# Kernel optimization log

Hardware: AMD Instinct MI355X
Metric: run time of the kernel (lower is better)

## Reference

```python
import jax, jax.numpy as jnp
import numpy as np

B, Q, H, NH, HD = 2, 1024, 2048, 16, 128
QKV_ALPHA = 1e-4   # W8A8B8O8Linear output scale (a)
QKV_BETA = 1.0     # W8A8B8O8Linear bias scale (b)
QK_SCALE = 1e-4    # BMM_S8T_S8N_F32T dequant scale
PV_SCALE = 2e-3    # BMM_S8T_S8N_S8T output scale
DENSE_ALPHA = 1e-5 # W8A8BFP32OFP32Linear dequant scale
INV_NORM = 1.0 / (HD ** 0.5)


def setup_inputs() -> dict:
    key = jax.random.key(0)
    ks = jax.random.split(key, 8)
    hidden_states = jax.random.randint(ks[0], (B, Q, H), -128, 128, dtype=jnp.int32)  # int8 activations
    residual = jax.random.normal(ks[1], (B, Q, H), dtype=jnp.float32)
    alibi = jax.random.normal(ks[2], (B * NH, 1, Q), dtype=jnp.float32) * 0.1
    causal = jnp.triu(jnp.ones((Q, Q), dtype=bool), k=1)  # True = masked (future positions)
    attention_mask = jnp.broadcast_to(causal[None, None], (B, 1, Q, Q))
    w_qkv = jax.random.randint(ks[3], (3 * H, H), -128, 128, dtype=jnp.int32)   # int8 weight
    b_qkv = jax.random.randint(ks[4], (3 * H,), -128, 128, dtype=jnp.int32)     # int8 bias
    w_dense = jax.random.randint(ks[5], (H, H), -128, 128, dtype=jnp.int32)     # int8 weight
    b_dense = jax.random.normal(ks[6], (H,), dtype=jnp.float32)                 # fp32 bias
    return dict(hidden_states=hidden_states, residual=residual, alibi=alibi,
                attention_mask=attention_mask, w_qkv=w_qkv, b_qkv=b_qkv,
                w_dense=w_dense, b_dense=b_dense)


def _quant_i8(x_f32):
    return jnp.clip(jnp.round(x_f32), -128, 127).astype(jnp.int32)


def reference(hidden_states, residual, alibi, attention_mask, w_qkv, b_qkv, w_dense, b_dense):
    # --- W8A8B8O8 fused QKV linear: int8 in, int8 out ---
    acc = jnp.einsum('bqh,oh->bqo', hidden_states, w_qkv)  # exact int32 accumulation
    fused_qkv = _quant_i8(acc.astype(jnp.float32) * QKV_ALPHA + b_qkv.astype(jnp.float32) * QKV_BETA)
    # _split_heads: [B,Q,3H] -> [B,Q,NH,3,HD]
    qkv = fused_qkv.reshape(B, Q, NH, 3, HD)
    q = qkv[..., 0, :].transpose(0, 2, 1, 3).reshape(B * NH, Q, HD)
    k = qkv[..., 1, :].transpose(0, 2, 1, 3).reshape(B * NH, Q, HD)
    v = qkv[..., 2, :].transpose(0, 2, 1, 3).reshape(B * NH, Q, HD)
    # --- BMM_S8T_S8N_F32T: int8 q @ k^T -> fp32 * scale, plus alibi bias ---
    scores_i32 = jnp.einsum('nqd,nkd->nqk', q, k)  # [B*NH,Q,KV] int32
    matmul_result = alibi * 1.0 + scores_i32.astype(jnp.float32) * QK_SCALE * INV_NORM
    attention_scores = matmul_result.reshape(B, NH, Q, Q)
    # masked softmax (True = masked)
    attn_weights = jnp.where(attention_mask, jnp.finfo(jnp.float32).min, attention_scores)
    attention_probs = jax.nn.softmax(attn_weights, axis=-1)
    # quantize probs to int8 with scale 1/127 (BMM_S8T_S8N_S8T A-side)
    p_i8 = _quant_i8(attention_probs * 127.0).reshape(B * NH, Q, Q)
    # --- BMM_S8T_S8N_S8T: int8 probs @ int8 v -> int8 context ---
    ctx_acc = jnp.einsum('nqk,nkd->nqd', p_i8, v)  # int32
    ctx_i8 = _quant_i8(ctx_acc.astype(jnp.float32) * PV_SCALE)
    # _merge_heads: [B*NH,Q,HD] -> [B,Q,H]
    ctx = ctx_i8.reshape(B, NH, Q, HD).transpose(0, 2, 1, 3).reshape(B, Q, H)
    # --- W8A8BFP32OFP32 dense: int8 in, fp32 out ---
    dense_acc = jnp.einsum('bqh,oh->bqo', ctx, w_dense)
    output = dense_acc.astype(jnp.float32) * DENSE_ALPHA + b_dense + residual
    return output
```

## Files before the change

### kernel.cpp

```cpp
#include <hip/hip_runtime.h>
#include <stdint.h>

typedef int i32x4 __attribute__((ext_vector_type(4)));

#define DEV __device__ __forceinline__

DEV void glds16(const void* g, void* l) {
  __builtin_amdgcn_global_load_lds(
      (const __attribute__((address_space(1))) void*)g,
      (__attribute__((address_space(3))) void*)l, 16, 0, 0);
}

DEV int clampi8(float f) {
  int v = (int)rintf(f);
  return v < -128 ? -128 : (v > 127 ? 127 : v);
}

__global__ void pack_kernel(const int* __restrict__ src, int8_t* __restrict__ dst, int n4) {
  int i = blockIdx.x * blockDim.x + threadIdx.x;
  if (i < n4) {
    int4 v = ((const int4*)src)[i];
    char4 c;
    c.x = (char)v.x; c.y = (char)v.y; c.z = (char)v.z; c.w = (char)v.w;
    ((char4*)dst)[i] = c;
  }
}

template<int K>
DEV void gemm_core(const int8_t* __restrict__ A, const int8_t* __restrict__ B,
                   int row0, int col0, i32x4 acc[4][4], char* lA, char* lB,
                   int l, int w, int wm, int wn) {
  const int lr = l & 15, lg = l >> 4;
  for (int k0 = 0; k0 < K; k0 += 64) {
    __syncthreads();
#pragma unroll
    for (int t = 0; t < 2; ++t) {
      const int mb = w * 2 + t;
      glds16(A + (size_t)(row0 + mb * 16 + lr) * K + k0 + lg * 16, lA + mb * 1024);
      glds16(B + (size_t)(col0 + mb * 16 + lr) * K + k0 + lg * 16, lB + mb * 1024);
    }
    __syncthreads();
    i32x4 a[4], b[4];
#pragma unroll
    for (int i = 0; i < 4; ++i) a[i] = *(const i32x4*)(lA + ((wm * 4 + i) * 64 + l) * 16);
#pragma unroll
    for (int j = 0; j < 4; ++j) b[j] = *(const i32x4*)(lB + ((wn * 4 + j) * 64 + l) * 16);
#pragma unroll
    for (int i = 0; i < 4; ++i)
#pragma unroll
      for (int j = 0; j < 4; ++j)
        acc[i][j] = __builtin_amdgcn_mfma_i32_16x16x64_i8(a[i], b[j], acc[i][j], 0, 0, 0);
  }
}

__global__ __launch_bounds__(256) void qkv_kernel(
    const int8_t* __restrict__ hs8, const int8_t* __restrict__ w8,
    const int* __restrict__ bq, int8_t* __restrict__ qb, int8_t* __restrict__ kb,
    int8_t* __restrict__ vT) {
  __shared__ __align__(16) char lA[8192];
  __shared__ __align__(16) char lB[8192];
  const int l = threadIdx.x & 63, w = threadIdx.x >> 6;
  const int wm = w >> 1, wn = w & 1;
  const int lr = l & 15, lg = l >> 4;
  const int row0 = blockIdx.y * 128, col0 = blockIdx.x * 128;
  i32x4 acc[4][4] = {};
  gemm_core<2048>(hs8, w8, row0, col0, acc, lA, lB, l, w, wm, wn);
#pragma unroll
  for (int j = 0; j < 4; ++j) {
    const int col = col0 + (wn * 4 + j) * 16 + lr;
    const float bias = (float)bq[col];
    const int nh = col / 384, rem = col - nh * 384;
    const int s = rem >> 7, d = rem & 127;
#pragma unroll
    for (int i = 0; i < 4; ++i) {
#pragma unroll
      for (int r = 0; r < 4; ++r) {
        const int row = row0 + (wm * 4 + i) * 16 + lg * 4 + r;
        const int bb = row >> 10, qpos = row & 1023;
        const int n = bb * 16 + nh;
        const int8_t c = (int8_t)clampi8((float)acc[i][j][r] * 1e-4f + bias);
        if (s == 0)      qb[((size_t)n << 17) + (qpos << 7) + d] = c;
        else if (s == 1) kb[((size_t)n << 17) + (qpos << 7) + d] = c;
        else             vT[((size_t)n << 17) + (d << 10) + qpos] = c;
      }
    }
  }
}

__global__ __launch_bounds__(256) void attn_stats_kernel(
    const int8_t* __restrict__ qb, const int8_t* __restrict__ kb,
    const float* __restrict__ alibi, float* __restrict__ stats) {
  __shared__ __align__(16) char lQ[16384];
  __shared__ __align__(16) char lK[16384];
  const int n = blockIdx.y;
  const int tri = blockIdx.x;
  int qt = 0;
  while ((qt + 1) * (qt + 2) / 2 <= tri) ++qt;
  const int kt = tri - qt * (qt + 1) / 2;
  const int l = threadIdx.x & 63, w = threadIdx.x >> 6;
  const int lr = l & 15, lg = l >> 4;
  const int row0 = qt * 128;
  const int8_t* Qh = qb + ((size_t)n << 17);
  const int8_t* Kh = kb + ((size_t)n << 17);
  const float* al = alibi + n * 1024;

#pragma unroll
  for (int e0 = 0; e0 < 4; ++e0) {
    const int e = w * 4 + e0, ks = e >> 3, mb = e & 7;
    glds16(Qh + (size_t)(row0 + mb * 16 + lr) * 128 + ks * 64 + lg * 16, lQ + e * 1024);
    glds16(Kh + (size_t)(kt * 128 + mb * 16 + lr) * 128 + ks * 64 + lg * 16, lK + e * 1024);
  }
  __syncthreads();
  i32x4 qa[2][2];
#pragma unroll
  for (int t = 0; t < 2; ++t)
#pragma unroll
    for (int ks = 0; ks < 2; ++ks)
      qa[t][ks] = *(const i32x4*)(lQ + (ks * 8 + w * 2 + t) * 1024 + l * 16);

  float sf[2][8][4];
#pragma unroll
  for (int nf = 0; nf < 8; ++nf) {
    const i32x4 bk0 = *(const i32x4*)(lK + nf * 1024 + l * 16);
    const i32x4 bk1 = *(const i32x4*)(lK + (8 + nf) * 1024 + l * 16);
    const int col = kt * 128 + nf * 16 + lr;
    const float av = al[col];
#pragma unroll
    for (int t = 0; t < 2; ++t) {
      i32x4 sa = {0, 0, 0, 0};
      sa = __builtin_amdgcn_mfma_i32_16x16x64_i8(qa[t][0], bk0, sa, 0, 0, 0);
      sa = __builtin_amdgcn_mfma_i32_16x16x64_i8(qa[t][1], bk1, sa, 0, 0, 0);
#pragma unroll
      for (int r = 0; r < 4; ++r) {
        const int rowg = row0 + (w * 2 + t) * 16 + lg * 4 + r;
        sf[t][nf][r] = (col <= rowg)
            ? av + ((float)sa[r] * 1e-4f) * 0.08838834764831843f
            : -INFINITY;
      }
    }
  }
#pragma unroll
  for (int t = 0; t < 2; ++t)
#pragma unroll
    for (int r = 0; r < 4; ++r) {
      float tm = sf[t][0][r];
#pragma unroll
      for (int nf = 1; nf < 8; ++nf) tm = fmaxf(tm, sf[t][nf][r]);
#pragma unroll
      for (int o = 1; o < 16; o <<= 1) tm = fmaxf(tm, __shfl_xor(tm, o));
      float es = 0.f;
#pragma unroll
      for (int nf = 0; nf < 8; ++nf) es += __expf(sf[t][nf][r] - tm);
#pragma unroll
      for (int o = 1; o < 16; o <<= 1) es += __shfl_xor(es, o);
      if (lr == 0) {
        const int rowl = (w * 2 + t) * 16 + lg * 4 + r;
        float2* st = (float2*)stats;
        st[((n * 8 + qt) * 8 + kt) * 128 + rowl] = make_float2(tm, es);
      }
    }
}

__global__ __launch_bounds__(256) void attn_pv_kernel(
    const int8_t* __restrict__ qb, const int8_t* __restrict__ kb,
    const int8_t* __restrict__ vT, const float* __restrict__ alibi,
    const float* __restrict__ stats, int* __restrict__ slab0,
    int* __restrict__ slab1, int8_t* __restrict__ ctx) {
  __shared__ __align__(16) char lQ[16384];
  __shared__ __align__(16) char lK[16384];
  __shared__ __align__(16) char lV[16384];
  __shared__ __align__(16) char lP[128 * 144];
  const int n = blockIdx.y, gi = blockIdx.x;
  int qt, g, kt0, kt1;
  if (gi < 4) { qt = gi; g = 0; kt0 = 0; kt1 = qt + 1; }
  else { const int p = gi - 4; qt = 4 + (p >> 1); g = p & 1; kt0 = g ? 4 : 0; kt1 = g ? qt + 1 : 4; }
  const int l = threadIdx.x & 63, w = threadIdx.x >> 6;
  const int lr = l & 15, lg = l >> 4;
  const int row0 = qt * 128;
  const int8_t* Qh = qb + ((size_t)n << 17);
  const int8_t* Kh = kb + ((size_t)n << 17);
  const int8_t* Vh = vT + ((size_t)n << 17);
  const float* al = alibi + n * 1024;

#pragma unroll
  for (int e0 = 0; e0 < 4; ++e0) {
    const int e = w * 4 + e0, ks = e >> 3, mb = e & 7;
    glds16(Qh + (size_t)(row0 + mb * 16 + lr) * 128 + ks * 64 + lg * 16, lQ + e * 1024);
  }
  __syncthreads();
  i32x4 qa[2][2];
#pragma unroll
  for (int t = 0; t < 2; ++t)
#pragma unroll
    for (int ks = 0; ks < 2; ++ks)
      qa[t][ks] = *(const i32x4*)(lQ + (ks * 8 + w * 2 + t) * 1024 + l * 16);

  float mrow[2][4], srow[2][4];
  const float2* st = (const float2*)stats;
#pragma unroll
  for (int t = 0; t < 2; ++t)
#pragma unroll
    for (int r = 0; r < 4; ++r) {
      const int rowl = (w * 2 + t) * 16 + lg * 4 + r;
      const int base = ((n * 8 + qt) * 8) * 128 + rowl;
      float m = -INFINITY;
      for (int k2 = 0; k2 <= qt; ++k2) m = fmaxf(m, st[base + k2 * 128].x);
      float s = 0.f;
      for (int k2 = 0; k2 <= qt; ++k2) {
        const float2 p = st[base + k2 * 128];
        s += p.y * __expf(p.x - m);
      }
      mrow[t][r] = m; srow[t][r] = s;
    }

  i32x4 pacc[2][8] = {};
  for (int kt = kt0; kt < kt1; ++kt) {
    __syncthreads();
#pragma unroll
    for (int e0 = 0; e0 < 4; ++e0) {
      const int e = w * 4 + e0, ks = e >> 3, mb = e & 7;
      glds16(Kh + (size_t)(kt * 128 + mb * 16 + lr) * 128 + ks * 64 + lg * 16, lK + e * 1024);
      glds16(Vh + (size_t)(mb * 16 + lr) * 1024 + kt * 128 + ks * 64 + lg * 16, lV + e * 1024);
    }
    __syncthreads();
#pragma unroll
    for (int nf = 0; nf < 8; ++nf) {
      const i32x4 bk0 = *(const i32x4*)(lK + nf * 1024 + l * 16);
      const i32x4 bk1 = *(const i32x4*)(lK + (8 + nf) * 1024 + l * 16);
      const int col = kt * 128 + nf * 16 + lr;
      const float av = al[col];
#pragma unroll
      for (int t = 0; t < 2; ++t) {
        i32x4 sa = {0, 0, 0, 0};
        sa = __builtin_amdgcn_mfma_i32_16x16x64_i8(qa[t][0], bk0, sa, 0, 0, 0);
        sa = __builtin_amdgcn_mfma_i32_16x16x64_i8(qa[t][1], bk1, sa, 0, 0, 0);
#pragma unroll
        for (int r = 0; r < 4; ++r) {
          const int rowl = (w * 2 + t) * 16 + lg * 4 + r;
          const int rowg = row0 + rowl;
          int p = 0;
          if (col <= rowg) {
            const float s = av + ((float)sa[r] * 1e-4f) * 0.08838834764831843f;
            p = (int)rintf(__expf(s - mrow[t][r]) / srow[t][r] * 127.0f);
          }
          lP[rowl * 144 + nf * 16 + lr] = (char)p;
        }
      }
    }
    __syncthreads();
#pragma unroll
    for (int t = 0; t < 2; ++t) {
      const int rowl = (w * 2 + t) * 16 + lr;
      const i32x4 pa0 = *(const i32x4*)(lP + rowl * 144 + lg * 16);
      const i32x4 pa1 = *(const i32x4*)(lP + rowl * 144 + 64 + lg * 16);
#pragma unroll
      for (int nf = 0; nf < 8; ++nf) {
        const i32x4 vb0 = *(const i32x4*)(lV + nf * 1024 + l * 16);
        const i32x4 vb1 = *(const i32x4*)(lV + (8 + nf) * 1024 + l * 16);
        pacc[t][nf] = __builtin_amdgcn_mfma_i32_16x16x64_i8(pa0, vb0, pacc[t][nf], 0, 0, 0);
        pacc[t][nf] = __builtin_amdgcn_mfma_i32_16x16x64_i8(pa1, vb1, pacc[t][nf], 0, 0, 0);
      }
    }
  }
  const int bb = n >> 4, nh = n & 15;
  if (qt < 4) {
#pragma unroll
    for (int t = 0; t < 2; ++t)
#pragma unroll
      for (int nf = 0; nf < 8; ++nf)
#pragma unroll
        for (int r = 0; r < 4; ++r) {
          const int qpos = row0 + (w * 2 + t) * 16 + lg * 4 + r;
          const int d = nf * 16 + lr;
          ctx[((size_t)(bb * 1024 + qpos)) * 2048 + nh * 128 + d] =
              (int8_t)clampi8((float)pacc[t][nf][r] * 2e-3f);
        }
  } else {
    int* slab = g ? slab1 : slab0;
#pragma unroll
    for (int t = 0; t < 2; ++t)
#pragma unroll
      for (int nf = 0; nf < 8; ++nf)
#pragma unroll
        for (int r = 0; r < 4; ++r) {
          const int qpos = row0 + (w * 2 + t) * 16 + lg * 4 + r;
          const int d = nf * 16 + lr;
          slab[(size_t)(bb * 512 + qpos - 512) * 2048 + nh * 128 + d] = pacc[t][nf][r];
        }
  }
}

__global__ void ctx_reduce_kernel(const int* __restrict__ slab0,
                                  const int* __restrict__ slab1,
                                  int8_t* __restrict__ ctx) {
  const int i = blockIdx.x * blockDim.x + threadIdx.x;
  const int4 a = ((const int4*)slab0)[i];
  const int4 b = ((const int4*)slab1)[i];
  const int elem0 = i * 4;
  const int r512 = elem0 >> 11, col = elem0 & 2047;
  const int bb = r512 >> 9, qpos = 512 + (r512 & 511);
  char4 c;
  c.x = (char)clampi8((float)(a.x + b.x) * 2e-3f);
  c.y = (char)clampi8((float)(a.y + b.y) * 2e-3f);
  c.z = (char)clampi8((float)(a.z + b.z) * 2e-3f);
  c.w = (char)clampi8((float)(a.w + b.w) * 2e-3f);
  ((char4*)ctx)[((size_t)(bb * 1024 + qpos) * 2048 + col) >> 2] = c;
}

__global__ __launch_bounds__(256) void dense_kernel(
    const int8_t* __restrict__ c8, const int8_t* __restrict__ w8,
    const float* __restrict__ bd, const float* __restrict__ res,
    float* __restrict__ out) {
  __shared__ __align__(16) char lA[8192];
  __shared__ __align__(16) char lB[8192];
  const int l = threadIdx.x & 63, w = threadIdx.x >> 6;
  const int wm = w >> 1, wn = w & 1;
  const int lr = l & 15, lg = l >> 4;
  const int row0 = blockIdx.y * 128, col0 = blockIdx.x * 128;
  i32x4 acc[4][4] = {};
  gemm_core<2048>(c8, w8, row0, col0, acc, lA, lB, l, w, wm, wn);
#pragma unroll
  for (int j = 0; j < 4; ++j) {
    const int col = col0 + (wn * 4 + j) * 16 + lr;
    const float bias = bd[col];
#pragma unroll
    for (int i = 0; i < 4; ++i) {
#pragma unroll
      for (int r = 0; r < 4; ++r) {
        const int row = row0 + (wm * 4 + i) * 16 + lg * 4 + r;
        const size_t o = (size_t)row * 2048 + col;
        out[o] = (float)acc[i][j][r] * 1e-5f + bias + res[o];
      }
    }
  }
}

extern "C" void kernel_launch(void* const* d_in, const int* in_sizes, int n_in,
                              void* d_out, int out_size, void* d_ws, size_t ws_size,
                              hipStream_t stream) {
  const int* hs = (const int*)d_in[0];
  const float* res = (const float*)d_in[1];
  const float* alibi = (const float*)d_in[2];
  const int* wqkv = (const int*)d_in[4];
  const int* bqkv = (const int*)d_in[5];
  const int* wd = (const int*)d_in[6];
  const float* bd = (const float*)d_in[7];
  float* out = (float*)d_out;
  char* ws = (char*)d_ws;

  int8_t* hs8   = (int8_t*)(ws + 0);
  int8_t* wqkv8 = (int8_t*)(ws + 4194304);
  int*    slab0 = (int*)(ws + 0);
  int*    slab1 = (int*)(ws + 8388608);
  int8_t* wd8   = (int8_t*)(ws + 16777216);
  int8_t* q8b   = (int8_t*)(ws + 20971520);
  int8_t* k8b   = (int8_t*)(ws + 25165824);
  int8_t* vT8   = (int8_t*)(ws + 29360128);
  int8_t* ctx8  = (int8_t*)(ws + 33554432);
  float*  stats = (float*)(ws + 37748736);

  pack_kernel<<<4096, 256, 0, stream>>>(hs, hs8, 1048576);
  pack_kernel<<<12288, 256, 0, stream>>>(wqkv, wqkv8, 3145728);
  pack_kernel<<<4096, 256, 0, stream>>>(wd, wd8, 1048576);
  qkv_kernel<<<dim3(48, 16), 256, 0, stream>>>(hs8, wqkv8, bqkv, q8b, k8b, vT8);
  attn_stats_kernel<<<dim3(36, 32), 256, 0, stream>>>(q8b, k8b, alibi, stats);
  attn_pv_kernel<<<dim3(12, 32), 256, 0, stream>>>(q8b, k8b, vT8, alibi, stats,
                                                   slab0, slab1, ctx8);
  ctx_reduce_kernel<<<2048, 256, 0, stream>>>(slab0, slab1, ctx8);
  dense_kernel<<<dim3(16, 16), 256, 0, stream>>>(ctx8, wd8, bd, res, out);
}
```

Baseline: 189.5 us.

## Double-buffer GEMM loads, fuse pack kernels, drop LDS staging in attention

The shared GEMM core now double-buffers its LDS tiles: it prefetches the next K-slice with global_load_lds while computing on the current one, leaving one barrier per iteration instead of two. The dense GEMM moves to a 128x64 tile with its own double-buffered loop, giving twice as many blocks. The three int32-to-int8 pack launches merge into one kernel. The attention kernels load Q, K and V fragments straight from global memory into registers instead of staging them through LDS. That removes barriers and LDS traffic but relies on cache hits for the repeated strided reads.

```diff
diff --git a/kernel.cpp b/kernel.cpp
--- a/kernel.cpp
+++ b/kernel.cpp
@@ -16,14 +16,20 @@
   return v < -128 ? -128 : (v > 127 ? 127 : v);
 }
 
-__global__ void pack_kernel(const int* __restrict__ src, int8_t* __restrict__ dst, int n4) {
-  int i = blockIdx.x * blockDim.x + threadIdx.x;
-  if (i < n4) {
-    int4 v = ((const int4*)src)[i];
-    char4 c;
-    c.x = (char)v.x; c.y = (char)v.y; c.z = (char)v.z; c.w = (char)v.w;
-    ((char4*)dst)[i] = c;
-  }
+__global__ void pack_all_kernel(const int* __restrict__ s0, const int* __restrict__ s1,
+                                const int* __restrict__ s2, int8_t* __restrict__ d0,
+                                int8_t* __restrict__ d1, int8_t* __restrict__ d2) {
+  const int i = blockIdx.x * 256 + threadIdx.x;
+  const int* s;
+  int8_t* d;
+  int j;
+  if (i < 1048576) { s = s0; d = d0; j = i; }
+  else if (i < 4194304) { s = s1; d = d1; j = i - 1048576; }
+  else { s = s2; d = d2; j = i - 4194304; }
+  int4 v = ((const int4*)s)[j];
+  char4 c;
+  c.x = (char)v.x; c.y = (char)v.y; c.z = (char)v.z; c.w = (char)v.w;
+  ((char4*)d)[j] = c;
 }
 
 template<int K>
@@ -31,25 +37,38 @@
                    int row0, int col0, i32x4 acc[4][4], char* lA, char* lB,
                    int l, int w, int wm, int wn) {
   const int lr = l & 15, lg = l >> 4;
+  const int8_t* pA0 = A + (size_t)(row0 + (w * 2 + 0) * 16 + lr) * K + lg * 16;
+  const int8_t* pA1 = A + (size_t)(row0 + (w * 2 + 1) * 16 + lr) * K + lg * 16;
+  const int8_t* pB0 = B + (size_t)(col0 + (w * 2 + 0) * 16 + lr) * K + lg * 16;
+  const int8_t* pB1 = B + (size_t)(col0 + (w * 2 + 1) * 16 + lr) * K + lg * 16;
+  glds16(pA0, lA + (w * 2 + 0) * 1024);
+  glds16(pA1, lA + (w * 2 + 1) * 1024);
+  glds16(pB0, lB + (w * 2 + 0) * 1024);
+  glds16(pB1, lB + (w * 2 + 1) * 1024);
+  __syncthreads();
+  int cur = 0;
   for (int k0 = 0; k0 < K; k0 += 64) {
-    __syncthreads();
-#pragma unroll
-    for (int t = 0; t < 2; ++t) {
-      const int mb = w * 2 + t;
-      glds16(A + (size_t)(row0 + mb * 16 + lr) * K + k0 + lg * 16, lA + mb * 1024);
-      glds16(B + (size_t)(col0 + mb * 16 + lr) * K + k0 + lg * 16, lB + mb * 1024);
-    }
-    __syncthreads();
+    const int nxt = cur ^ 1;
+    if (k0 + 64 < K) {
+      glds16(pA0 + k0 + 64, lA + nxt * 8192 + (w * 2 + 0) * 1024);
+      glds16(pA1 + k0 + 64, lA + nxt * 8192 + (w * 2 + 1) * 1024);
+      glds16(pB0 + k0 + 64, lB + nxt * 8192 + (w * 2 + 0) * 1024);
+      glds16(pB1 + k0 + 64, lB + nxt * 8192 + (w * 2 + 1) * 1024);
+    }
     i32x4 a[4], b[4];
 #pragma unroll
-    for (int i = 0; i < 4; ++i) a[i] = *(const i32x4*)(lA + ((wm * 4 + i) * 64 + l) * 16);
-#pragma unroll
-    for (int j = 0; j < 4; ++j) b[j] = *(const i32x4*)(lB + ((wn * 4 + j) * 64 + l) * 16);
+    for (int i = 0; i < 4; ++i)
+      a[i] = *(const i32x4*)(lA + cur * 8192 + ((wm * 4 + i) * 64 + l) * 16);
+#pragma unroll
+    for (int j = 0; j < 4; ++j)
+      b[j] = *(const i32x4*)(lB + cur * 8192 + ((wn * 4 + j) * 64 + l) * 16);
 #pragma unroll
     for (int i = 0; i < 4; ++i)
 #pragma unroll
       for (int j = 0; j < 4; ++j)
         acc[i][j] = __builtin_amdgcn_mfma_i32_16x16x64_i8(a[i], b[j], acc[i][j], 0, 0, 0);
+    __syncthreads();
+    cur = nxt;
   }
 }
 
@@ -57,8 +76,8 @@
     const int8_t* __restrict__ hs8, const int8_t* __restrict__ w8,
     const int* __restrict__ bq, int8_t* __restrict__ qb, int8_t* __restrict__ kb,
     int8_t* __restrict__ vT) {
-  __shared__ __align__(16) char lA[8192];
-  __shared__ __align__(16) char lB[8192];
+  __shared__ __align__(16) char lA[16384];
+  __shared__ __align__(16) char lB[16384];
   const int l = threadIdx.x & 63, w = threadIdx.x >> 6;
   const int wm = w >> 1, wn = w & 1;
   const int lr = l & 15, lg = l >> 4;
@@ -90,8 +109,6 @@
 __global__ __launch_bounds__(256) void attn_stats_kernel(
     const int8_t* __restrict__ qb, const int8_t* __restrict__ kb,
     const float* __restrict__ alibi, float* __restrict__ stats) {
-  __shared__ __align__(16) char lQ[16384];
-  __shared__ __align__(16) char lK[16384];
   const int n = blockIdx.y;
   const int tri = blockIdx.x;
   int qt = 0;
@@ -104,25 +121,19 @@
   const int8_t* Kh = kb + ((size_t)n << 17);
   const float* al = alibi + n * 1024;
 
-#pragma unroll
-  for (int e0 = 0; e0 < 4; ++e0) {
-    const int e = w * 4 + e0, ks = e >> 3, mb = e & 7;
-    glds16(Qh + (size_t)(row0 + mb * 16 + lr) * 128 + ks * 64 + lg * 16, lQ + e * 1024);
-    glds16(Kh + (size_t)(kt * 128 + mb * 16 + lr) * 128 + ks * 64 + lg * 16, lK + e * 1024);
-  }
-  __syncthreads();
   i32x4 qa[2][2];
 #pragma unroll
   for (int t = 0; t < 2; ++t)
 #pragma unroll
     for (int ks = 0; ks < 2; ++ks)
-      qa[t][ks] = *(const i32x4*)(lQ + (ks * 8 + w * 2 + t) * 1024 + l * 16);
+      qa[t][ks] = *(const i32x4*)(Qh + (size_t)(row0 + (w * 2 + t) * 16 + lr) * 128 + ks * 64 + lg * 16);
 
   float sf[2][8][4];
 #pragma unroll
   for (int nf = 0; nf < 8; ++nf) {
-    const i32x4 bk0 = *(const i32x4*)(lK + nf * 1024 + l * 16);
-    const i32x4 bk1 = *(const i32x4*)(lK + (8 + nf) * 1024 + l * 16);
+    const size_t krow = (size_t)(kt * 128 + nf * 16 + lr) * 128;
+    const i32x4 bk0 = *(const i32x4*)(Kh + krow + lg * 16);
+    const i32x4 bk1 = *(const i32x4*)(Kh + krow + 64 + lg * 16);
     const int col = kt * 128 + nf * 16 + lr;
     const float av = al[col];
 #pragma unroll
@@ -166,9 +177,6 @@
     const int8_t* __restrict__ vT, const float* __restrict__ alibi,
     const float* __restrict__ stats, int* __restrict__ slab0,
     int* __restrict__ slab1, int8_t* __restrict__ ctx) {
-  __shared__ __align__(16) char lQ[16384];
-  __shared__ __align__(16) char lK[16384];
-  __shared__ __align__(16) char lV[16384];
   __shared__ __align__(16) char lP[128 * 144];
   const int n = blockIdx.y, gi = blockIdx.x;
   int qt, g, kt0, kt1;
@@ -182,18 +190,12 @@
   const int8_t* Vh = vT + ((size_t)n << 17);
   const float* al = alibi + n * 1024;
 
-#pragma unroll
-  for (int e0 = 0; e0 < 4; ++e0) {
-    const int e = w * 4 + e0, ks = e >> 3, mb = e & 7;
-    glds16(Qh + (size_t)(row0 + mb * 16 + lr) * 128 + ks * 64 + lg * 16, lQ + e * 1024);
-  }
-  __syncthreads();
   i32x4 qa[2][2];
 #pragma unroll
   for (int t = 0; t < 2; ++t)
 #pragma unroll
     for (int ks = 0; ks < 2; ++ks)
-      qa[t][ks] = *(const i32x4*)(lQ + (ks * 8 + w * 2 + t) * 1024 + l * 16);
+      qa[t][ks] = *(const i32x4*)(Qh + (size_t)(row0 + (w * 2 + t) * 16 + lr) * 128 + ks * 64 + lg * 16);
 
   float mrow[2][4], srow[2][4];
   const float2* st = (const float2*)stats;
@@ -215,18 +217,11 @@
 
   i32x4 pacc[2][8] = {};
   for (int kt = kt0; kt < kt1; ++kt) {
-    __syncthreads();
-#pragma unroll
-    for (int e0 = 0; e0 < 4; ++e0) {
-      const int e = w * 4 + e0, ks = e >> 3, mb = e & 7;
-      glds16(Kh + (size_t)(kt * 128 + mb * 16 + lr) * 128 + ks * 64 + lg * 16, lK + e * 1024);
-      glds16(Vh + (size_t)(mb * 16 + lr) * 1024 + kt * 128 + ks * 64 + lg * 16, lV + e * 1024);
-    }
-    __syncthreads();
 #pragma unroll
     for (int nf = 0; nf < 8; ++nf) {
-      const i32x4 bk0 = *(const i32x4*)(lK + nf * 1024 + l * 16);
-      const i32x4 bk1 = *(const i32x4*)(lK + (8 + nf) * 1024 + l * 16);
+      const size_t krow = (size_t)(kt * 128 + nf * 16 + lr) * 128;
+      const i32x4 bk0 = *(const i32x4*)(Kh + krow + lg * 16);
+      const i32x4 bk1 = *(const i32x4*)(Kh + krow + 64 + lg * 16);
       const int col = kt * 128 + nf * 16 + lr;
       const float av = al[col];
 #pragma unroll
@@ -255,8 +250,9 @@
       const i32x4 pa1 = *(const i32x4*)(lP + rowl * 144 + 64 + lg * 16);
 #pragma unroll
       for (int nf = 0; nf < 8; ++nf) {
-        const i32x4 vb0 = *(const i32x4*)(lV + nf * 1024 + l * 16);
-        const i32x4 vb1 = *(const i32x4*)(lV + (8 + nf) * 1024 + l * 16);
+        const size_t vrow = (size_t)(nf * 16 + lr) * 1024 + kt * 128;
+        const i32x4 vb0 = *(const i32x4*)(Vh + vrow + lg * 16);
+        const i32x4 vb1 = *(const i32x4*)(Vh + vrow + 64 + lg * 16);
         pacc[t][nf] = __builtin_amdgcn_mfma_i32_16x16x64_i8(pa0, vb0, pacc[t][nf], 0, 0, 0);
         pacc[t][nf] = __builtin_amdgcn_mfma_i32_16x16x64_i8(pa1, vb1, pacc[t][nf], 0, 0, 0);
       }
@@ -311,17 +307,46 @@
     const int8_t* __restrict__ c8, const int8_t* __restrict__ w8,
     const float* __restrict__ bd, const float* __restrict__ res,
     float* __restrict__ out) {
-  __shared__ __align__(16) char lA[8192];
+  __shared__ __align__(16) char lA[16384];
   __shared__ __align__(16) char lB[8192];
   const int l = threadIdx.x & 63, w = threadIdx.x >> 6;
   const int wm = w >> 1, wn = w & 1;
   const int lr = l & 15, lg = l >> 4;
-  const int row0 = blockIdx.y * 128, col0 = blockIdx.x * 128;
-  i32x4 acc[4][4] = {};
-  gemm_core<2048>(c8, w8, row0, col0, acc, lA, lB, l, w, wm, wn);
-#pragma unroll
-  for (int j = 0; j < 4; ++j) {
-    const int col = col0 + (wn * 4 + j) * 16 + lr;
+  const int row0 = blockIdx.y * 128, col0 = blockIdx.x * 64;
+  const int8_t* pA0 = c8 + (size_t)(row0 + (w * 2 + 0) * 16 + lr) * 2048 + lg * 16;
+  const int8_t* pA1 = c8 + (size_t)(row0 + (w * 2 + 1) * 16 + lr) * 2048 + lg * 16;
+  const int8_t* pB  = w8 + (size_t)(col0 + w * 16 + lr) * 2048 + lg * 16;
+  glds16(pA0, lA + (w * 2 + 0) * 1024);
+  glds16(pA1, lA + (w * 2 + 1) * 1024);
+  glds16(pB,  lB + w * 1024);
+  __syncthreads();
+  i32x4 acc[4][2] = {};
+  int cur = 0;
+  for (int k0 = 0; k0 < 2048; k0 += 64) {
+    const int nxt = cur ^ 1;
+    if (k0 + 64 < 2048) {
+      glds16(pA0 + k0 + 64, lA + nxt * 8192 + (w * 2 + 0) * 1024);
+      glds16(pA1 + k0 + 64, lA + nxt * 8192 + (w * 2 + 1) * 1024);
+      glds16(pB + k0 + 64, lB + nxt * 4096 + w * 1024);
+    }
+    i32x4 a[4], b[2];
+#pragma unroll
+    for (int i = 0; i < 4; ++i)
+      a[i] = *(const i32x4*)(lA + cur * 8192 + ((wm * 4 + i) * 64 + l) * 16);
+#pragma unroll
+    for (int j = 0; j < 2; ++j)
+      b[j] = *(const i32x4*)(lB + cur * 4096 + ((wn * 2 + j) * 64 + l) * 16);
+#pragma unroll
+    for (int i = 0; i < 4; ++i)
+#pragma unroll
+      for (int j = 0; j < 2; ++j)
+        acc[i][j] = __builtin_amdgcn_mfma_i32_16x16x64_i8(a[i], b[j], acc[i][j], 0, 0, 0);
+    __syncthreads();
+    cur = nxt;
+  }
+#pragma unroll
+  for (int j = 0; j < 2; ++j) {
+    const int col = col0 + (wn * 2 + j) * 16 + lr;
     const float bias = bd[col];
 #pragma unroll
     for (int i = 0; i < 4; ++i) {
@@ -359,13 +384,11 @@
   int8_t* ctx8  = (int8_t*)(ws + 33554432);
   float*  stats = (float*)(ws + 37748736);
 
-  pack_kernel<<<4096, 256, 0, stream>>>(hs, hs8, 1048576);
-  pack_kernel<<<12288, 256, 0, stream>>>(wqkv, wqkv8, 3145728);
-  pack_kernel<<<4096, 256, 0, stream>>>(wd, wd8, 1048576);
+  pack_all_kernel<<<20480, 256, 0, stream>>>(hs, wqkv, wd, hs8, wqkv8, wd8);
   qkv_kernel<<<dim3(48, 16), 256, 0, stream>>>(hs8, wqkv8, bqkv, q8b, k8b, vT8);
   attn_stats_kernel<<<dim3(36, 32), 256, 0, stream>>>(q8b, k8b, alibi, stats);
   attn_pv_kernel<<<dim3(12, 32), 256, 0, stream>>>(q8b, k8b, vT8, alibi, stats,
                                                    slab0, slab1, ctx8);
   ctx_reduce_kernel<<<2048, 256, 0, stream>>>(slab0, slab1, ctx8);
-  dense_kernel<<<dim3(16, 16), 256, 0, stream>>>(ctx8, wd8, bd, res, out);
-}
+  dense_kernel<<<dim3(32, 16), 256, 0, stream>>>(ctx8, wd8, bd, res, out);
+}
```

Measured after the change: 197.6 us. 1.04x slower.
